# Optimization experiments

Measured on AMD Instinct MI355X. Metric: run time of the kernel, lower is better.

## Reference

```python
import jax, jax.numpy as jnp
import numpy as np

B = 100_000   # graph nodes in batch
C = 1_000     # virtual-node clusters
D = 512       # in_dim (attention hidden dim)
OUT = 512     # out_dim


def setup_inputs() -> dict:
    key = jax.random.key(0)
    ks = jax.random.split(key, 9)
    h = jax.random.normal(ks[0], (B, D), dtype=jnp.float32)
    g = jax.random.normal(ks[1], (C, D), dtype=jnp.float32)
    # vn_index[:,1] is the cluster id of node i; arange%C guarantees every
    # cluster is present, so the per-cluster concat has exactly C rows in
    # sorted-cluster-id order (matching torch .unique() iteration order).
    vn_index = jnp.stack([jnp.arange(B, dtype=jnp.int32),
                          jnp.arange(B, dtype=jnp.int32) % C], axis=1)
    n_id = jnp.arange(B, dtype=jnp.int32)
    s = 1.0 / np.sqrt(D)
    Wq = jax.random.uniform(ks[2], (D, D), jnp.float32, -s, s)   # query_proj (no bias)
    Wk = jax.random.uniform(ks[3], (D, D), jnp.float32, -s, s)   # key_proj (no bias)
    attn_bias = jax.random.uniform(ks[4], (D,), jnp.float32, -0.1, 0.1)
    Ws = jax.random.uniform(ks[5], (1, D), jnp.float32, -s, s)   # score_proj weight
    bs = jax.random.uniform(ks[6], (1,), jnp.float32, -s, s)     # score_proj bias
    so = 1.0 / np.sqrt(D)
    W = jax.random.uniform(ks[7], (OUT, D), jnp.float32, -so, so)  # final Linear
    b = jax.random.uniform(ks[8], (OUT,), jnp.float32, -so, so)
    return {"h": h, "g": g, "vn_index": vn_index, "n_id": n_id,
            "Wq": Wq, "Wk": Wk, "attn_bias": attn_bias, "Ws": Ws, "bs": bs,
            "W": W, "b": b}


def reference(h, g, vn_index, n_id, Wq, Wk, attn_bias, Ws, bs, W, b):
    # cluster id for each batch node (B,)
    cluster = vn_index[n_id, 1]
    # additive attention, vectorized over all nodes (replaces per-cluster loop)
    qp = g @ Wq.T                                   # (C, D) query proj per cluster
    kp = h @ Wk.T                                   # (B, D) key proj per node
    score = jnp.tanh(kp + qp[cluster] + attn_bias) @ Ws[0] + bs[0]  # (B,)
    # segment softmax over each cluster
    smax = jax.ops.segment_max(score, cluster, num_segments=C)      # (C,)
    e = jnp.exp(score - smax[cluster])                              # (B,)
    denom = jax.ops.segment_sum(e, cluster, num_segments=C)         # (C,)
    attn = e / denom[cluster]                                       # (B,)
    # attention-weighted sum of node features per cluster -> (C, D)
    ctx = jax.ops.segment_sum(attn[:, None] * h, cluster, num_segments=C)
    # final projection + tanh activation -> (C, OUT)
    return jnp.tanh(ctx @ W.T + b)
```

## Files before the change

### kernel.cpp

```cpp
#include <hip/hip_runtime.h>
#include <stdint.h>

#define D_DIM 512

typedef __attribute__((ext_vector_type(8))) short bf16x8;
typedef __attribute__((ext_vector_type(4))) float f32x4;
typedef __attribute__((ext_vector_type(4))) short short4_t;
typedef __attribute__((ext_vector_type(4))) float float4_t;

__device__ __forceinline__ unsigned short f2bf(float f) {
  unsigned u = __float_as_uint(f);
  u += 0x7FFFu + ((u >> 16) & 1u);
  return (unsigned short)(u >> 16);
}

__device__ __forceinline__ float bf2f(unsigned short s) {
  return __uint_as_float(((unsigned)s) << 16);
}

__device__ __forceinline__ float tanh_fast(float x) {
  float e = __expf(2.0f * x);
  return 1.0f - 2.0f / (e + 1.0f);
}

#define GLOAD_LDS16(gsrc, ldst) \
  __builtin_amdgcn_global_load_lds((const __attribute__((address_space(1))) void*)(gsrc), \
                                   (__attribute__((address_space(3))) void*)(ldst), 16, 0, 0)


__global__ void cvt_f32_bf16_k(const float* __restrict__ in, unsigned short* __restrict__ out, int n4) {
  int i = blockIdx.x * blockDim.x + threadIdx.x;
  if (i < n4) {
    float4_t v = ((const float4_t*)in)[i];
    short4_t s;
    s.x = (short)f2bf(v.x); s.y = (short)f2bf(v.y);
    s.z = (short)f2bf(v.z); s.w = (short)f2bf(v.w);
    ((short4_t*)out)[i] = s;
  }
}

__global__ void prep_cluster_k(const int* __restrict__ vn, const int* __restrict__ nid,
                               int* __restrict__ cl, int* __restrict__ counts, int B) {
  int i = blockIdx.x * blockDim.x + threadIdx.x;
  if (i < B) {
    int c = vn[2 * nid[i] + 1];
    cl[i] = c;
    atomicAdd(&counts[c], 1);
  }
}

__global__ void prefix_k(const int* __restrict__ counts, int* __restrict__ starts,
                         int* __restrict__ cursor, int C) {
  __shared__ int sh[1024];
  int t = threadIdx.x;
  int v = (t < C) ? counts[t] : 0;
  sh[t] = v;
  __syncthreads();
  for (int off = 1; off < 1024; off <<= 1) {
    int x = (t >= off) ? sh[t - off] : 0;
    __syncthreads();
    sh[t] += x;
    __syncthreads();
  }
  if (t < C) { int st = sh[t] - v; starts[t] = st; cursor[t] = st; }
  if (t == 1023) starts[C] = sh[1023];
}

__global__ void scatter_k(const int* __restrict__ cl, int* __restrict__ cursor,
                          int* __restrict__ order, int B) {
  int i = blockIdx.x * blockDim.x + threadIdx.x;
  if (i < B) {
    int pos = atomicAdd(&cursor[cl[i]], 1);
    order[pos] = i;
  }
}

__device__ __forceinline__ unsigned enc_f(float f) {
  unsigned u = __float_as_uint(f);
  return (u & 0x80000000u) ? ~u : (u | 0x80000000u);
}
__device__ __forceinline__ float dec_f(unsigned u) {
  return __uint_as_float((u & 0x80000000u) ? (u & 0x7FFFFFFFu) : ~u);
}

__global__ void seg_max_k(const float* __restrict__ score, const int* __restrict__ cl,
                          unsigned* __restrict__ smax, int B) {
  int i = blockIdx.x * blockDim.x + threadIdx.x;
  if (i < B) atomicMax(&smax[cl[i]], enc_f(score[i]));
}

__global__ void seg_expsum_k(const float* __restrict__ score, const int* __restrict__ cl,
                             const unsigned* __restrict__ smax, float* __restrict__ ev,
                             float* __restrict__ denom, int B) {
  int i = blockIdx.x * blockDim.x + threadIdx.x;
  if (i < B) {
    int c = cl[i];
    float x = __expf(score[i] - dec_f(smax[c]));
    ev[i] = x;
    atomicAdd(&denom[c], x);
  }
}

__global__ __launch_bounds__(512)
void ctx_k(const unsigned short* __restrict__ hbf, const float* __restrict__ ev,
           const int* __restrict__ order, const int* __restrict__ starts,
           const float* __restrict__ denom, float* __restrict__ ctx) {
  int c = blockIdx.x;
  int d = threadIdx.x;
  int s0 = starts[c], s1 = starts[c + 1];
  float acc = 0.f;
  int j = s0;
  for (; j + 1 < s1; j += 2) {
    int i0 = order[j], i1 = order[j + 1];
    float e0 = ev[i0], e1 = ev[i1];
    float h0 = bf2f(hbf[(size_t)i0 * D_DIM + d]);
    float h1 = bf2f(hbf[(size_t)i1 * D_DIM + d]);
    acc += e0 * h0 + e1 * h1;
  }
  if (j < s1) {
    int i0 = order[j];
    acc += ev[i0] * bf2f(hbf[(size_t)i0 * D_DIM + d]);
  }
  ctx[(size_t)c * D_DIM + d] = acc / denom[c];
}

template<int EPI>
__global__ __launch_bounds__(256)
void gemm128_k(const unsigned short* __restrict__ Abf,
               const unsigned short* __restrict__ Bw, int M,
               const float* __restrict__ qb, const int* __restrict__ cl,
               const float* __restrict__ Ws, const float* __restrict__ bias,
               float* __restrict__ out)
{
  __shared__ unsigned short As[128 * 64];
  __shared__ unsigned short Bs[128 * 64];
  __shared__ float red[128][2];
  __shared__ int clds[128];

  const int t = threadIdx.x;
  const int lane = t & 63;
  const int w = t >> 6;
  const int wr = w >> 1, wc = w & 1;
  const int l15 = lane & 15, l4 = lane >> 4;
  const int n0 = blockIdx.x * 128;
  const int m0 = blockIdx.y * 128;

  if (EPI == 1 && t < 128) {
    int gm = m0 + t;
    clds[t] = (gm < M) ? cl[gm] : 0;
  }

  const int rin = lane >> 3;
  const int sl = lane & 7;

  const unsigned short* srcA[4];
  const unsigned short* srcB[4];
  char* dstA[4];
  char* dstB[4];
  #pragma unroll
  for (int c = 0; c < 4; ++c) {
    int chunk = w * 4 + c;
    int row = chunk * 8 + rin;
    int slot = sl ^ (row & 7);
    int ga = m0 + row; if (ga > M - 1) ga = M - 1;
    srcA[c] = Abf + (size_t)ga * 512 + slot * 8;
    srcB[c] = Bw + (size_t)(n0 + row) * 512 + slot * 8;
    dstA[c] = ((char*)As) + chunk * 1024;
    dstB[c] = ((char*)Bs) + chunk * 1024;
  }

  int offA[4][2], offB[4][2];
  #pragma unroll
  for (int mi = 0; mi < 4; ++mi) {
    int row = wr * 64 + mi * 16 + l15;
    #pragma unroll
    for (int ks = 0; ks < 2; ++ks)
      offA[mi][ks] = row * 128 + (((ks * 4 + l4) ^ (row & 7)) * 16);
  }
  #pragma unroll
  for (int ni = 0; ni < 4; ++ni) {
    int row = wc * 64 + ni * 16 + l15;
    #pragma unroll
    for (int ks = 0; ks < 2; ++ks)
      offB[ni][ks] = row * 128 + (((ks * 4 + l4) ^ (row & 7)) * 16);
  }

  f32x4 acc[4][4];
  #pragma unroll
  for (int mi = 0; mi < 4; ++mi)
    #pragma unroll
    for (int ni = 0; ni < 4; ++ni)
      acc[mi][ni] = (f32x4){0.f, 0.f, 0.f, 0.f};

  for (int k0 = 0; k0 < 512; k0 += 64) {
    #pragma unroll
    for (int c = 0; c < 4; ++c) {
      GLOAD_LDS16(srcA[c] + k0, dstA[c]);
      GLOAD_LDS16(srcB[c] + k0, dstB[c]);
    }
    __syncthreads();

    #pragma unroll
    for (int ks = 0; ks < 2; ++ks) {
      bf16x8 af[4], bfv[4];
      #pragma unroll
      for (int mi = 0; mi < 4; ++mi)
        af[mi] = *(const bf16x8*)(((const char*)As) + offA[mi][ks]);
      #pragma unroll
      for (int ni = 0; ni < 4; ++ni)
        bfv[ni] = *(const bf16x8*)(((const char*)Bs) + offB[ni][ks]);
      #pragma unroll
      for (int mi = 0; mi < 4; ++mi)
        #pragma unroll
        for (int ni = 0; ni < 4; ++ni)
          acc[mi][ni] = __builtin_amdgcn_mfma_f32_16x16x32_bf16(af[mi], bfv[ni], acc[mi][ni], 0, 0, 0);
    }
    __syncthreads();
  }

  if (EPI == 0 || EPI == 2) {
    #pragma unroll
    for (int mi = 0; mi < 4; ++mi) {
      #pragma unroll
      for (int r = 0; r < 4; ++r) {
        int gm = m0 + wr * 64 + mi * 16 + l4 * 4 + r;
        if (gm < M) {
          #pragma unroll
          for (int ni = 0; ni < 4; ++ni) {
            int gcol = n0 + wc * 64 + ni * 16 + l15;
            float v = acc[mi][ni][r] + bias[gcol];
            if (EPI == 2) v = tanh_fast(v);
            out[(size_t)gm * 512 + gcol] = v;
          }
        }
      }
    }
  } else {
    #pragma unroll
    for (int mi = 0; mi < 4; ++mi) {
      #pragma unroll
      for (int r = 0; r < 4; ++r) {
        int rowt = wr * 64 + mi * 16 + l4 * 4 + r;
        int c = clds[rowt];
        const float* qrow = &qb[(size_t)c * 512 + n0 + wc * 64];
        float s = 0.f;
        #pragma unroll
        for (int ni = 0; ni < 4; ++ni) {
          int colw = ni * 16 + l15;
          float x = acc[mi][ni][r] + qrow[colw];
          s += tanh_fast(x) * Ws[n0 + wc * 64 + colw];
        }
        s += __shfl_xor(s, 1);
        s += __shfl_xor(s, 2);
        s += __shfl_xor(s, 4);
        s += __shfl_xor(s, 8);
        if (l15 == 0) red[rowt][wc] = s;
      }
    }
    __syncthreads();
    if (t < 128) {
      int gm = m0 + t;
      if (gm < M) atomicAdd(&out[gm], red[t][0] + red[t][1]);
    }
  }
}


extern "C" void kernel_launch(void* const* d_in, const int* in_sizes, int n_in,
                              void* d_out, int out_size, void* d_ws, size_t ws_size,
                              hipStream_t stream) {
  const float* h  = (const float*)d_in[0];
  const float* g  = (const float*)d_in[1];
  const int*   vn = (const int*)d_in[2];
  const int*   nid= (const int*)d_in[3];
  const float* Wq = (const float*)d_in[4];
  const float* Wk = (const float*)d_in[5];
  const float* ab = (const float*)d_in[6];
  const float* Ws = (const float*)d_in[7];
  const float* W  = (const float*)d_in[9];
  const float* b  = (const float*)d_in[10];

  const int B = in_sizes[3];
  const int C = in_sizes[1] / D_DIM;

  char* wsb = (char*)d_ws;
  size_t off = 0;
  auto alloc = [&](size_t bytes) -> void* {
    void* p = wsb + off;
    off += (bytes + 255) & ~(size_t)255;
    return p;
  };

  unsigned short* hbf   = (unsigned short*)alloc((size_t)B * 512 * 2);
  unsigned short* gbf   = (unsigned short*)alloc((size_t)C * 512 * 2);
  unsigned short* ctxbf = (unsigned short*)alloc((size_t)C * 512 * 2);
  unsigned short* Wk_bf = (unsigned short*)alloc((size_t)512 * 512 * 2);
  unsigned short* Wq_bf = (unsigned short*)alloc((size_t)512 * 512 * 2);
  unsigned short* W_bf  = (unsigned short*)alloc((size_t)512 * 512 * 2);
  float* qb    = (float*)alloc((size_t)C * 512 * 4);
  float* ctx   = (float*)alloc((size_t)C * 512 * 4);
  float* score = (float*)alloc((size_t)B * 4);
  float* ev    = (float*)alloc((size_t)B * 4);
  int*   cl    = (int*)alloc((size_t)B * 4);
  int*   order = (int*)alloc((size_t)B * 4);
  int*      counts = (int*)alloc((size_t)C * 4);
  unsigned* smax   = (unsigned*)alloc((size_t)C * 4);
  float*    denom  = (float*)alloc((size_t)C * 4);
  int* starts = (int*)alloc((size_t)(C + 1) * 4);
  int* cursor = (int*)alloc((size_t)C * 4);
  (void)ws_size; (void)n_in; (void)out_size;

  size_t zlen = (size_t)((char*)denom - (char*)counts) + (size_t)C * 4;
  hipMemsetAsync(counts, 0, zlen, stream);
  hipMemsetAsync(score, 0, (size_t)B * 4, stream);

  cvt_f32_bf16_k<<<(B * 512 / 4 + 255) / 256, 256, 0, stream>>>(h, hbf, B * 512 / 4);
  cvt_f32_bf16_k<<<(C * 512 / 4 + 255) / 256, 256, 0, stream>>>(g, gbf, C * 512 / 4);
  const int n4w = 512 * 512 / 4;
  cvt_f32_bf16_k<<<(n4w + 255) / 256, 256, 0, stream>>>(Wk, Wk_bf, n4w);
  cvt_f32_bf16_k<<<(n4w + 255) / 256, 256, 0, stream>>>(Wq, Wq_bf, n4w);
  cvt_f32_bf16_k<<<(n4w + 255) / 256, 256, 0, stream>>>(W, W_bf, n4w);

  prep_cluster_k<<<(B + 255) / 256, 256, 0, stream>>>(vn, nid, cl, counts, B);
  prefix_k<<<1, 1024, 0, stream>>>(counts, starts, cursor, C);
  scatter_k<<<(B + 255) / 256, 256, 0, stream>>>(cl, cursor, order, B);

  gemm128_k<0><<<dim3(4, (C + 127) / 128), 256, 0, stream>>>(
      gbf, Wq_bf, C, nullptr, nullptr, nullptr, ab, qb);

  gemm128_k<1><<<dim3(4, (B + 127) / 128), 256, 0, stream>>>(
      hbf, Wk_bf, B, qb, cl, Ws, nullptr, score);

  seg_max_k<<<(B + 255) / 256, 256, 0, stream>>>(score, cl, smax, B);
  seg_expsum_k<<<(B + 255) / 256, 256, 0, stream>>>(score, cl, smax, ev, denom, B);
  ctx_k<<<C, 512, 0, stream>>>(hbf, ev, order, starts, denom, ctx);

  cvt_f32_bf16_k<<<(C * 512 / 4 + 255) / 256, 256, 0, stream>>>(ctx, ctxbf, C * 512 / 4);

  gemm128_k<2><<<dim3(4, (C + 127) / 128), 256, 0, stream>>>(
      ctxbf, W_bf, C, nullptr, nullptr, nullptr, b, (float*)d_out);
}
```

Before: 265.6 us.

## Double-buffer GEMM LDS loads, remap workgroups across XCDs, vectorize ctx, merge weight casts

The GEMM now keeps two LDS stages, so the global-to-LDS loads for the next K slice are issued before the MFMAs on the current slice. It also switches to a 1D grid with an XCD-aware workgroup remap. The context kernel uses 256 threads that each load two bf16 values, with a 4-way unrolled loop. The three weight conversions become a single launch. This aims to hide memory latency and reduce launch overhead, at the cost of doubled LDS per block, which may lower occupancy. The cvt3 kernel writes three contiguous outputs starting at Wk_bf, which is only correct if Wq_bf and W_bf sit right after it in memory.

```diff
diff --git a/kernel.cpp b/kernel.cpp
--- a/kernel.cpp
+++ b/kernel.cpp
@@ -37,6 +37,20 @@
     s.z = (short)f2bf(v.z); s.w = (short)f2bf(v.w);
     ((short4_t*)out)[i] = s;
   }
+}
+
+__global__ void cvt3_f32_bf16_k(const float* __restrict__ a, const float* __restrict__ b,
+                                const float* __restrict__ c, unsigned short* __restrict__ out,
+                                int n4each) {
+  int i = blockIdx.x * blockDim.x + threadIdx.x;
+  if (i >= 3 * n4each) return;
+  int sel = i / n4each, j = i - sel * n4each;
+  const float* src = (sel == 0) ? a : (sel == 1) ? b : c;
+  float4_t v = ((const float4_t*)src)[j];
+  short4_t s;
+  s.x = (short)f2bf(v.x); s.y = (short)f2bf(v.y);
+  s.z = (short)f2bf(v.z); s.w = (short)f2bf(v.w);
+  ((short4_t*)out)[i] = s;
 }
 
 __global__ void prep_cluster_k(const int* __restrict__ vn, const int* __restrict__ nid,
@@ -101,27 +115,37 @@
   }
 }
 
-__global__ __launch_bounds__(512)
+__global__ __launch_bounds__(256)
 void ctx_k(const unsigned short* __restrict__ hbf, const float* __restrict__ ev,
            const int* __restrict__ order, const int* __restrict__ starts,
            const float* __restrict__ denom, float* __restrict__ ctx) {
   int c = blockIdx.x;
-  int d = threadIdx.x;
+  int t = threadIdx.x;
   int s0 = starts[c], s1 = starts[c + 1];
-  float acc = 0.f;
+  float a0 = 0.f, a1 = 0.f;
   int j = s0;
-  for (; j + 1 < s1; j += 2) {
-    int i0 = order[j], i1 = order[j + 1];
-    float e0 = ev[i0], e1 = ev[i1];
-    float h0 = bf2f(hbf[(size_t)i0 * D_DIM + d]);
-    float h1 = bf2f(hbf[(size_t)i1 * D_DIM + d]);
-    acc += e0 * h0 + e1 * h1;
-  }
-  if (j < s1) {
+  for (; j + 3 < s1; j += 4) {
+    int i0 = order[j], i1 = order[j + 1], i2 = order[j + 2], i3 = order[j + 3];
+    float e0 = ev[i0], e1 = ev[i1], e2 = ev[i2], e3 = ev[i3];
+    unsigned u0 = *(const unsigned*)(hbf + (size_t)i0 * D_DIM + t * 2);
+    unsigned u1 = *(const unsigned*)(hbf + (size_t)i1 * D_DIM + t * 2);
+    unsigned u2 = *(const unsigned*)(hbf + (size_t)i2 * D_DIM + t * 2);
+    unsigned u3 = *(const unsigned*)(hbf + (size_t)i3 * D_DIM + t * 2);
+    a0 += e0 * bf2f((unsigned short)u0) + e1 * bf2f((unsigned short)u1)
+        + e2 * bf2f((unsigned short)u2) + e3 * bf2f((unsigned short)u3);
+    a1 += e0 * bf2f((unsigned short)(u0 >> 16)) + e1 * bf2f((unsigned short)(u1 >> 16))
+        + e2 * bf2f((unsigned short)(u2 >> 16)) + e3 * bf2f((unsigned short)(u3 >> 16));
+  }
+  for (; j < s1; ++j) {
     int i0 = order[j];
-    acc += ev[i0] * bf2f(hbf[(size_t)i0 * D_DIM + d]);
-  }
-  ctx[(size_t)c * D_DIM + d] = acc / denom[c];
+    float e0 = ev[i0];
+    unsigned u0 = *(const unsigned*)(hbf + (size_t)i0 * D_DIM + t * 2);
+    a0 += e0 * bf2f((unsigned short)u0);
+    a1 += e0 * bf2f((unsigned short)(u0 >> 16));
+  }
+  float inv = 1.0f / denom[c];
+  float2 r = make_float2(a0 * inv, a1 * inv);
+  *(float2*)(&ctx[(size_t)c * D_DIM + t * 2]) = r;
 }
 
 template<int EPI>
@@ -132,8 +156,8 @@
                const float* __restrict__ Ws, const float* __restrict__ bias,
                float* __restrict__ out)
 {
-  __shared__ unsigned short As[128 * 64];
-  __shared__ unsigned short Bs[128 * 64];
+  __shared__ unsigned short As[2][128 * 64];
+  __shared__ unsigned short Bs[2][128 * 64];
   __shared__ float red[128][2];
   __shared__ int clds[128];
 
@@ -142,8 +166,12 @@
   const int w = t >> 6;
   const int wr = w >> 1, wc = w & 1;
   const int l15 = lane & 15, l4 = lane >> 4;
-  const int n0 = blockIdx.x * 128;
-  const int m0 = blockIdx.y * 128;
+
+  const int nwg = gridDim.x;
+  int id = blockIdx.x;
+  if ((nwg & 7) == 0) id = (id & 7) * (nwg >> 3) + (id >> 3);
+  const int n0 = (id & 3) * 128;
+  const int m0 = (id >> 2) * 128;
 
   if (EPI == 1 && t < 128) {
     int gm = m0 + t;
@@ -155,8 +183,7 @@
 
   const unsigned short* srcA[4];
   const unsigned short* srcB[4];
-  char* dstA[4];
-  char* dstB[4];
+  int dstOff[4];
   #pragma unroll
   for (int c = 0; c < 4; ++c) {
     int chunk = w * 4 + c;
@@ -165,8 +192,7 @@
     int ga = m0 + row; if (ga > M - 1) ga = M - 1;
     srcA[c] = Abf + (size_t)ga * 512 + slot * 8;
     srcB[c] = Bw + (size_t)(n0 + row) * 512 + slot * 8;
-    dstA[c] = ((char*)As) + chunk * 1024;
-    dstB[c] = ((char*)Bs) + chunk * 1024;
+    dstOff[c] = chunk * 1024;
   }
 
   int offA[4][2], offB[4][2];
@@ -192,23 +218,33 @@
     for (int ni = 0; ni < 4; ++ni)
       acc[mi][ni] = (f32x4){0.f, 0.f, 0.f, 0.f};
 
-  for (int k0 = 0; k0 < 512; k0 += 64) {
-    #pragma unroll
-    for (int c = 0; c < 4; ++c) {
-      GLOAD_LDS16(srcA[c] + k0, dstA[c]);
-      GLOAD_LDS16(srcB[c] + k0, dstB[c]);
-    }
-    __syncthreads();
-
+  #pragma unroll
+  for (int c = 0; c < 4; ++c) {
+    GLOAD_LDS16(srcA[c], ((char*)As[0]) + dstOff[c]);
+    GLOAD_LDS16(srcB[c], ((char*)Bs[0]) + dstOff[c]);
+  }
+  __syncthreads();
+
+  #pragma unroll
+  for (int it = 0; it < 8; ++it) {
+    const int cur = it & 1;
+    if (it < 7) {
+      const int k1 = (it + 1) * 64;
+      #pragma unroll
+      for (int c = 0; c < 4; ++c) {
+        GLOAD_LDS16(srcA[c] + k1, ((char*)As[cur ^ 1]) + dstOff[c]);
+        GLOAD_LDS16(srcB[c] + k1, ((char*)Bs[cur ^ 1]) + dstOff[c]);
+      }
+    }
     #pragma unroll
     for (int ks = 0; ks < 2; ++ks) {
       bf16x8 af[4], bfv[4];
       #pragma unroll
       for (int mi = 0; mi < 4; ++mi)
-        af[mi] = *(const bf16x8*)(((const char*)As) + offA[mi][ks]);
+        af[mi] = *(const bf16x8*)(((const char*)As[cur]) + offA[mi][ks]);
       #pragma unroll
       for (int ni = 0; ni < 4; ++ni)
-        bfv[ni] = *(const bf16x8*)(((const char*)Bs) + offB[ni][ks]);
+        bfv[ni] = *(const bf16x8*)(((const char*)Bs[cur]) + offB[ni][ks]);
       #pragma unroll
       for (int mi = 0; mi < 4; ++mi)
         #pragma unroll
@@ -317,26 +353,24 @@
   cvt_f32_bf16_k<<<(B * 512 / 4 + 255) / 256, 256, 0, stream>>>(h, hbf, B * 512 / 4);
   cvt_f32_bf16_k<<<(C * 512 / 4 + 255) / 256, 256, 0, stream>>>(g, gbf, C * 512 / 4);
   const int n4w = 512 * 512 / 4;
-  cvt_f32_bf16_k<<<(n4w + 255) / 256, 256, 0, stream>>>(Wk, Wk_bf, n4w);
-  cvt_f32_bf16_k<<<(n4w + 255) / 256, 256, 0, stream>>>(Wq, Wq_bf, n4w);
-  cvt_f32_bf16_k<<<(n4w + 255) / 256, 256, 0, stream>>>(W, W_bf, n4w);
+  cvt3_f32_bf16_k<<<(3 * n4w + 255) / 256, 256, 0, stream>>>(Wk, Wq, W, Wk_bf, n4w);
 
   prep_cluster_k<<<(B + 255) / 256, 256, 0, stream>>>(vn, nid, cl, counts, B);
   prefix_k<<<1, 1024, 0, stream>>>(counts, starts, cursor, C);
   scatter_k<<<(B + 255) / 256, 256, 0, stream>>>(cl, cursor, order, B);
 
-  gemm128_k<0><<<dim3(4, (C + 127) / 128), 256, 0, stream>>>(
+  gemm128_k<0><<<4 * ((C + 127) / 128), 256, 0, stream>>>(
       gbf, Wq_bf, C, nullptr, nullptr, nullptr, ab, qb);
 
-  gemm128_k<1><<<dim3(4, (B + 127) / 128), 256, 0, stream>>>(
+  gemm128_k<1><<<4 * ((B + 127) / 128), 256, 0, stream>>>(
       hbf, Wk_bf, B, qb, cl, Ws, nullptr, score);
 
   seg_max_k<<<(B + 255) / 256, 256, 0, stream>>>(score, cl, smax, B);
   seg_expsum_k<<<(B + 255) / 256, 256, 0, stream>>>(score, cl, smax, ev, denom, B);
-  ctx_k<<<C, 512, 0, stream>>>(hbf, ev, order, starts, denom, ctx);
+  ctx_k<<<C, 256, 0, stream>>>(hbf, ev, order, starts, denom, ctx);
 
   cvt_f32_bf16_k<<<(C * 512 / 4 + 255) / 256, 256, 0, stream>>>(ctx, ctxbf, C * 512 / 4);
 
-  gemm128_k<2><<<dim3(4, (C + 127) / 128), 256, 0, stream>>>(
+  gemm128_k<2><<<4 * ((C + 127) / 128), 256, 0, stream>>>(
       ctxbf, W_bf, C, nullptr, nullptr, nullptr, b, (float*)d_out);
 }
```

After: 261.9 us. Within noise of the previous version (-1.4%).
